# Kernel optimization log

Measured on AMD Instinct MI355X. Metric: run time of the kernel, lower is better.

## Reference

```python
import jax, jax.numpy as jnp
import numpy as np

NUM_HEADS = 4   # forced by reshape(B, N, num_heads, C) of a dim*4 projection
BN_EPS = 1e-5


def _chamfer(a, b):
    # a, b: [B, N, 3] -> symmetric chamfer distance (mean of nearest sq-dists)
    d = (jnp.sum(a ** 2, -1)[:, :, None] + jnp.sum(b ** 2, -1)[:, None, :]
         - 2.0 * jnp.einsum('bnc,bmc->bnm', a, b))
    return jnp.mean(jnp.min(d, axis=2)) + jnp.mean(jnp.min(d, axis=1))


def _forward(xs, pc1, bn_gamma, bn_beta, q_w, kv_w, proj_w, proj_b, map_w, map_b):
    B, F, C, N = xs.shape
    H = NUM_HEADS
    scale = C ** -0.5  # head_dim == dim in this module (full-dim heads)

    def per_item(x):  # x: [F, C, N]
        # BatchNorm1d in eval mode (running_mean=0, running_var=1)
        xn = (x / jnp.sqrt(1.0 + BN_EPS)) * bn_gamma[:, None] + bn_beta[:, None]
        xn = xn.transpose(0, 2, 1)                 # [F, N, C]
        xr = xn[::-1]                              # flip over frame axis
        q = (xn @ q_w.T).reshape(F, N, H, C).transpose(0, 2, 1, 3)        # [F,H,N,C]
        kv = (xr @ kv_w.T).reshape(F, N, 2, H, C).transpose(2, 0, 3, 1, 4)
        k, v = kv[0], kv[1]                        # [F,H,N,C]
        attn = jax.nn.softmax(jnp.einsum('fhnc,fhmc->fhnm', q, k) * scale, axis=-1)
        o = jnp.einsum('fhnm,fhmc->fhnc', attn, v).transpose(0, 2, 1, 3)  # [F,N,H,C]
        xa = (o[0] + o[1]).transpose(1, 0, 2)      # [H, N, C]: sum of first two frames
        xa = xa @ proj_w.T + proj_b                # [H, N, C] x_appearance
        fr = xa @ map_w.T + map_b                  # [H, N, 3] frames (mapping_xyz)
        return xa, fr

    xa, frames = jax.vmap(per_item)(xs)            # [B,H,N,C], [B,H,N,3]
    pc1t = pc1.transpose(0, 2, 1)                  # [B, N, 3]
    loss = _chamfer(pc1t + frames[:, 0], pc1t)
    return xa[:, 1:], frames[:, 1:], loss


def setup_inputs() -> dict:
    key = jax.random.key(0)
    ks = jax.random.split(key, 8)
    B, F, C, N = 2, 4, 64, 2048
    return {
        'xs': jax.random.normal(ks[0], (B, F, C, N), jnp.float32),
        'pc1': jax.random.normal(ks[1], (B, 3, N), jnp.float32),
        'pc2': jax.random.normal(ks[2], (B, 3, N), jnp.float32),
        'bn_gamma': jnp.ones((C,), jnp.float32),
        'bn_beta': jnp.zeros((C,), jnp.float32),
        'q_w': 0.02 * jax.random.normal(ks[3], (4 * C, C), jnp.float32),
        'kv_w': 0.02 * jax.random.normal(ks[4], (8 * C, C), jnp.float32),
        'proj_w': 0.02 * jax.random.normal(ks[5], (C, C), jnp.float32),
        'proj_b': jnp.zeros((C,), jnp.float32),
        'map_w': 0.02 * jax.random.normal(ks[6], (3, C), jnp.float32),
        'map_b': jnp.zeros((3,), jnp.float32),
    }


def reference(xs, pc1, pc2, bn_gamma, bn_beta, q_w, kv_w, proj_w, proj_b, map_w, map_b):
    # pc2 is accepted by the torch forward but unused in its body
    return _forward(xs, pc1, bn_gamma, bn_beta, q_w, kv_w, proj_w, proj_b, map_w, map_b)
```

## Files before the change

kernel.cpp:

```cpp
#include <hip/hip_runtime.h>
#include <hip/hip_bf16.h>

#define NPTS 2048
#define LOG2E 1.4426950408889634f
#define NJC 16
#define JCH 128

typedef short bf16x8 __attribute__((ext_vector_type(8)));
typedef float f32x4 __attribute__((ext_vector_type(4)));
typedef unsigned uint32x4 __attribute__((ext_vector_type(4)));
typedef __attribute__((address_space(3))) char lds_char;
typedef __attribute__((address_space(1))) const char glob_char;

union PBU { uint32x4 u; bf16x8 v; };

static __device__ __forceinline__ unsigned cvt_pk_bf16(float a, float b) {
    unsigned r;
    asm("v_cvt_pk_bf16_f32 %0, %1, %2" : "=v"(r) : "v"(a), "v"(b));
    return r;
}

__global__ void prep_weights(const float* __restrict__ gamma, const float* __restrict__ beta,
                             const float* __restrict__ q_w, const float* __restrict__ kv_w,
                             float* __restrict__ Wp, float* __restrict__ bp) {
    int j = blockIdx.x * blockDim.x + threadIdx.x;
    if (j >= 768) return;
    const float inv = 1.0f / sqrtf(1.0f + 1e-5f);
    const float* src;
    float scale;
    if (j < 256) { src = q_w + j * 64;          scale = 0.125f * LOG2E; }
    else         { src = kv_w + (j - 256) * 64; scale = 1.0f; }
    float b = 0.f;
    for (int c = 0; c < 64; ++c) {
        float w = src[c];
        Wp[j * 64 + c] = w * gamma[c] * inv * scale;
        b += w * beta[c];
    }
    bp[j] = b * scale;
}

__global__ __launch_bounds__(256) void qkv_gemm(const float* __restrict__ xs,
                                                const float* __restrict__ Wp,
                                                const float* __restrict__ bp,
                                                __hip_bfloat16* __restrict__ Qg,
                                                __hip_bfloat16* __restrict__ Kg,
                                                __hip_bfloat16* __restrict__ Vtg) {
    const int bf = blockIdx.z;
    const int b = bf >> 1, f01 = bf & 1;
    const int jt = blockIdx.y;
    const int f_src = (jt < 4) ? f01 : (3 - f01);
    const int n0 = blockIdx.x * 64;
    const float* __restrict__ A = xs + (size_t)((b * 4 + f_src) * 64) * NPTS;

    __shared__ float As[64][68];
    __shared__ float Ws[64][68];

    const int t = threadIdx.x;
    const int tx = t & 15, ty = t >> 4;

    for (int r = 0; r < 4; ++r) {
        int row = ty + 16 * r;
        int col = tx * 4;
        *(float4*)&As[row][col] = *(const float4*)&A[(size_t)row * NPTS + n0 + col];
        *(float4*)&Ws[row][col] = *(const float4*)&Wp[(size_t)(jt * 64 + row) * 64 + col];
    }
    __syncthreads();

    float acc[4][4];
#pragma unroll
    for (int jj = 0; jj < 4; ++jj) {
        float bv = bp[jt * 64 + tx + 16 * jj];
#pragma unroll
        for (int i = 0; i < 4; ++i) acc[i][jj] = bv;
    }
    for (int c = 0; c < 64; ++c) {
        float a[4], w[4];
#pragma unroll
        for (int i = 0; i < 4; ++i) a[i] = As[c][ty + 16 * i];
#pragma unroll
        for (int jj = 0; jj < 4; ++jj) w[jj] = Ws[tx + 16 * jj][c];
#pragma unroll
        for (int i = 0; i < 4; ++i)
#pragma unroll
            for (int jj = 0; jj < 4; ++jj) acc[i][jj] += a[i] * w[jj];
    }

    if (jt < 8) {
        __hip_bfloat16* __restrict__ dst = (jt < 4 ? Qg : Kg) + (size_t)bf * NPTS * 256;
        const int jb = (jt & 3) * 64;
#pragma unroll
        for (int i = 0; i < 4; ++i) {
            int n = n0 + ty + 16 * i;
#pragma unroll
            for (int jj = 0; jj < 4; ++jj)
                dst[(size_t)n * 256 + jb + tx + 16 * jj] = __float2bfloat16(acc[i][jj]);
        }
    } else {
        __syncthreads();
#pragma unroll
        for (int i = 0; i < 4; ++i)
#pragma unroll
            for (int jj = 0; jj < 4; ++jj)
                As[tx + 16 * jj][ty + 16 * i] = acc[i][jj];
        __syncthreads();
        const int row = t >> 2, c0 = (t & 3) * 16;
        __hip_bfloat16* __restrict__ dst =
            Vtg + ((size_t)bf * 256 + (jt - 8) * 64 + row) * NPTS + n0 + c0;
#pragma unroll
        for (int c = 0; c < 16; ++c) dst[c] = __float2bfloat16(As[row][c0 + c]);
    }
}

__global__ __launch_bounds__(256) void attn_mfma(const __hip_bfloat16* __restrict__ Qg,
                                                 const __hip_bfloat16* __restrict__ Kg,
                                                 const __hip_bfloat16* __restrict__ Vtg,
                                                 float* __restrict__ OT,
                                                 float* __restrict__ Lp) {
    const int combo = blockIdx.x;
    const int bf = combo >> 2, h = combo & 3;
    const int n0 = blockIdx.y * 64;
    const int split = blockIdx.z;
    const int kbase = split * (NPTS / 2);
    const int NT = NPTS / 2 / 64;

    __shared__ __align__(16) char smem[32768];

    const int t = threadIdx.x;
    const int lane = t & 63, w = t >> 6;
    const int l15 = lane & 15, g = lane >> 4;
    const int srow = lane >> 3, sslot = lane & 7;

    const __hip_bfloat16* qbase =
        Qg + ((size_t)bf * NPTS + n0 + w * 16 + l15) * 256 + h * 64 + g * 8;
    bf16x8 qf0 = *(const bf16x8*)(qbase);
    bf16x8 qf1 = *(const bf16x8*)(qbase + 32);

    const __hip_bfloat16* kgb = Kg + (size_t)bf * NPTS * 256 + h * 64;
    const __hip_bfloat16* vgb = Vtg + ((size_t)bf * 256 + h * 64) * NPTS;

    f32x4 oacc[4];
    float lsum = 0.f;
#pragma unroll
    for (int r = 0; r < 4; ++r) oacc[r] = (f32x4){0.f, 0.f, 0.f, 0.f};

    auto stage = [&](int kt, int bsel) {
#pragma unroll
        for (int ii = 0; ii < 2; ++ii) {
            const int rb = w * 16 + ii * 8;
            const int r = rb + srow;
            const int cs = (sslot ^ (r & 7)) * 8;
            const __hip_bfloat16* ksrc = kgb + (size_t)(kbase + kt * 64 + r) * 256 + cs;
            __builtin_amdgcn_global_load_lds((const glob_char*)ksrc,
                (lds_char*)(smem + bsel * 16384 + rb * 128), 16, 0, 0);
            const __hip_bfloat16* vsrc = vgb + (size_t)r * NPTS + kbase + kt * 64 + cs;
            __builtin_amdgcn_global_load_lds((const glob_char*)vsrc,
                (lds_char*)(smem + bsel * 16384 + 8192 + rb * 128), 16, 0, 0);
        }
    };

    stage(0, 0);
    int cur = 0;

    for (int kt = 0; kt < NT; ++kt) {
        if (kt < NT - 1) {
            stage(kt + 1, cur ^ 1);
            asm volatile("s_waitcnt vmcnt(4)" ::: "memory");
        } else {
            asm volatile("s_waitcnt vmcnt(0)" ::: "memory");
        }
        __builtin_amdgcn_s_barrier();
        asm volatile("" ::: "memory");

        char* const Kt = smem + cur * 16384;
        char* const Vt = Kt + 8192;

        f32x4 st[4];
#pragma unroll
        for (int tt = 0; tt < 4; ++tt) {
            const int row = tt * 16 + l15;
            bf16x8 kf0 = *(const bf16x8*)(Kt + row * 128 + ((g ^ (row & 7)) << 4));
            bf16x8 kf1 = *(const bf16x8*)(Kt + row * 128 + (((4 + g) ^ (row & 7)) << 4));
            f32x4 z = (f32x4){0.f, 0.f, 0.f, 0.f};
            z = __builtin_amdgcn_mfma_f32_16x16x32_bf16(kf0, qf0, z, 0, 0, 0);
            z = __builtin_amdgcn_mfma_f32_16x16x32_bf16(kf1, qf1, z, 0, 0, 0);
            st[tt] = z;
        }

        unsigned c0[4], c1[4];
#pragma unroll
        for (int tt = 0; tt < 4; ++tt) {
            float p0 = exp2f(fminf(st[tt][0], 126.f));
            float p1 = exp2f(fminf(st[tt][1], 126.f));
            float p2 = exp2f(fminf(st[tt][2], 126.f));
            float p3 = exp2f(fminf(st[tt][3], 126.f));
            lsum += (p0 + p1) + (p2 + p3);
            c0[tt] = cvt_pk_bf16(p0, p1);
            c1[tt] = cvt_pk_bf16(p2, p3);
        }

        bf16x8 pb[2];
#pragma unroll
        for (int s = 0; s < 2; ++s) {
            unsigned x0 = c0[2 * s], y0 = c0[2 * s + 1];
            unsigned x1 = c1[2 * s], y1 = c1[2 * s + 1];
            asm("v_permlane32_swap_b32 %0, %1" : "+v"(x0), "+v"(y0));
            asm("v_permlane16_swap_b32 %0, %1" : "+v"(x0), "+v"(y0));
            asm("v_permlane32_swap_b32 %0, %1" : "+v"(x1), "+v"(y1));
            asm("v_permlane16_swap_b32 %0, %1" : "+v"(x1), "+v"(y1));
            PBU pu;
            pu.u = (uint32x4){x0, x1, y0, y1};
            pb[s] = pu.v;
        }

#pragma unroll
        for (int ct = 0; ct < 4; ++ct) {
            const int row = ct * 16 + l15;
            bf16x8 vf0 = *(const bf16x8*)(Vt + row * 128 + ((g ^ (row & 7)) << 4));
            bf16x8 vf1 = *(const bf16x8*)(Vt + row * 128 + (((4 + g) ^ (row & 7)) << 4));
            f32x4 z = oacc[ct];
            z = __builtin_amdgcn_mfma_f32_16x16x32_bf16(vf0, pb[0], z, 0, 0, 0);
            z = __builtin_amdgcn_mfma_f32_16x16x32_bf16(vf1, pb[1], z, 0, 0, 0);
            oacc[ct] = z;
        }

        asm volatile("s_waitcnt lgkmcnt(0)" ::: "memory");
        __builtin_amdgcn_s_barrier();
        asm volatile("" ::: "memory");
        cur ^= 1;
    }

    lsum += __shfl_xor(lsum, 16);
    lsum += __shfl_xor(lsum, 32);
    const int q = n0 + w * 16 + l15;
    if (g == 0)
        Lp[(size_t)(split * 16 + combo) * NPTS + q] = lsum;

    float* __restrict__ Op = OT + (size_t)(split * 16 + combo) * 64 * NPTS;
#pragma unroll
    for (int ct = 0; ct < 4; ++ct)
#pragma unroll
        for (int r = 0; r < 4; ++r)
            Op[(size_t)(ct * 16 + g * 4 + r) * NPTS + q] = oacc[ct][r];
}

__global__ __launch_bounds__(256) void proj_frames(const float* __restrict__ OT,
                                                   const float* __restrict__ Lp,
                                                   const float* __restrict__ proj_w,
                                                   const float* __restrict__ proj_b,
                                                   const float* __restrict__ map_w,
                                                   const float* __restrict__ map_b,
                                                   float* __restrict__ out,
                                                   float* __restrict__ frames0) {
    const int bh = blockIdx.y, b = bh >> 2, h = bh & 3;
    const int n0 = blockIdx.x * 64;
    const int cf0 = (b * 2 + 0) * 4 + h;
    const int cf1 = (b * 2 + 1) * 4 + h;

    __shared__ float Xs[64][68];
    __shared__ float Ws[64][68];
    __shared__ float xaS[64][68];

    const int t = threadIdx.x;
    const int tx = t & 15, ty = t >> 4;
    const int nc = n0 + tx * 4;

    float4 la = *(const float4*)&Lp[(size_t)cf0 * NPTS + nc];
    float4 lb = *(const float4*)&Lp[(size_t)(16 + cf0) * NPTS + nc];
    float4 inv0 = make_float4(1.f / (la.x + lb.x), 1.f / (la.y + lb.y),
                              1.f / (la.z + lb.z), 1.f / (la.w + lb.w));
    la = *(const float4*)&Lp[(size_t)cf1 * NPTS + nc];
    lb = *(const float4*)&Lp[(size_t)(16 + cf1) * NPTS + nc];
    float4 inv1 = make_float4(1.f / (la.x + lb.x), 1.f / (la.y + lb.y),
                              1.f / (la.z + lb.z), 1.f / (la.w + lb.w));

    for (int r = 0; r < 4; ++r) {
        int row = ty + 16 * r, col = tx * 4;
        const float* p00 = OT + ((size_t)(cf0)      * 64 + row) * NPTS + n0 + col;
        const float* p01 = OT + ((size_t)(16 + cf0) * 64 + row) * NPTS + n0 + col;
        const float* p10 = OT + ((size_t)(cf1)      * 64 + row) * NPTS + n0 + col;
        const float* p11 = OT + ((size_t)(16 + cf1) * 64 + row) * NPTS + n0 + col;
        float4 a0 = *(const float4*)p00, a1 = *(const float4*)p01;
        float4 b0 = *(const float4*)p10, b1 = *(const float4*)p11;
        float4 x;
        x.x = (a0.x + a1.x) * inv0.x + (b0.x + b1.x) * inv1.x;
        x.y = (a0.y + a1.y) * inv0.y + (b0.y + b1.y) * inv1.y;
        x.z = (a0.z + a1.z) * inv0.z + (b0.z + b1.z) * inv1.z;
        x.w = (a0.w + a1.w) * inv0.w + (b0.w + b1.w) * inv1.w;
        *(float4*)&Xs[row][col] = x;
        *(float4*)&Ws[row][col] = *(const float4*)&proj_w[(size_t)row * 64 + col];
    }
    __syncthreads();

    float acc[4][4];
#pragma unroll
    for (int jj = 0; jj < 4; ++jj) {
        float bv = proj_b[tx + 16 * jj];
#pragma unroll
        for (int i = 0; i < 4; ++i) acc[i][jj] = bv;
    }
    for (int c = 0; c < 64; ++c) {
        float a[4], w[4];
#pragma unroll
        for (int i = 0; i < 4; ++i) a[i] = Xs[c][ty + 16 * i];
#pragma unroll
        for (int jj = 0; jj < 4; ++jj) w[jj] = Ws[tx + 16 * jj][c];
#pragma unroll
        for (int i = 0; i < 4; ++i)
#pragma unroll
            for (int jj = 0; jj < 4; ++jj) acc[i][jj] += a[i] * w[jj];
    }

#pragma unroll
    for (int i = 0; i < 4; ++i)
#pragma unroll
        for (int jj = 0; jj < 4; ++jj)
            xaS[ty + 16 * i][tx + 16 * jj] = acc[i][jj];

    if (h >= 1) {
        float* __restrict__ xa_out = out + (size_t)(b * 3 + h - 1) * NPTS * 64;
#pragma unroll
        for (int i = 0; i < 4; ++i)
#pragma unroll
            for (int jj = 0; jj < 4; ++jj)
                xa_out[(size_t)(n0 + ty + 16 * i) * 64 + tx + 16 * jj] = acc[i][jj];
    }
    __syncthreads();

    if (t < 192) {
        int r = t / 3, j = t % 3;
        float s = map_b[j];
        for (int c = 0; c < 64; ++c) s += xaS[r][c] * map_w[j * 64 + c];
        int n = n0 + r;
        if (h == 0) frames0[((size_t)b * NPTS + n) * 3 + j] = s;
        else        out[786432 + ((size_t)(b * 3 + h - 1) * NPTS + n) * 3 + j] = s;
    }
}

__global__ __launch_bounds__(256) void chamfer_partial(const float* __restrict__ pc1,
                                                       const float* __restrict__ frames0,
                                                       float* __restrict__ partial) {
    const int z = blockIdx.z;
    const int dir = z >> 1, b = z & 1;
    const int i = blockIdx.x * 256 + threadIdx.x;
    const int j0 = blockIdx.y * JCH;
    const float* __restrict__ px = pc1 + (size_t)b * 3 * NPTS;
    const float* __restrict__ fr = frames0 + (size_t)b * NPTS * 3;

    __shared__ float4 sj[JCH];
    if (threadIdx.x < JCH) {
        int jj = j0 + threadIdx.x;
        float bx = px[jj], by = px[NPTS + jj], bz = px[2 * NPTS + jj];
        if (dir == 1) { bx += fr[jj * 3]; by += fr[jj * 3 + 1]; bz += fr[jj * 3 + 2]; }
        sj[threadIdx.x] = make_float4(bx, by, bz, bx * bx + by * by + bz * bz);
    }
    float ax = px[i], ay = px[NPTS + i], az = px[2 * NPTS + i];
    if (dir == 0) { ax += fr[i * 3]; ay += fr[i * 3 + 1]; az += fr[i * 3 + 2]; }
    const float a2 = ax * ax + ay * ay + az * az;
    __syncthreads();

    float best = 1e30f;
#pragma unroll 4
    for (int k = 0; k < JCH; ++k) {
        float4 p = sj[k];
        float d = a2 + p.w - 2.0f * (ax * p.x + ay * p.y + az * p.z);
        best = fminf(best, d);
    }
    partial[((size_t)z * NJC + blockIdx.y) * NPTS + i] = best;
}

__global__ __launch_bounds__(256) void chamfer_minsum(const float* __restrict__ partial,
                                                      double* __restrict__ sums) {
    const int gid = blockIdx.x * 256 + threadIdx.x;
    const int z = gid >> 11, i = gid & 2047;
    float best = 1e30f;
#pragma unroll
    for (int c = 0; c < NJC; ++c)
        best = fminf(best, partial[((size_t)z * NJC + c) * NPTS + i]);
    __shared__ double sm[256];
    sm[threadIdx.x] = (double)best;
    __syncthreads();
    for (int off = 128; off > 0; off >>= 1) {
        if (threadIdx.x < off) sm[threadIdx.x] += sm[threadIdx.x + off];
        __syncthreads();
    }
    if (threadIdx.x == 0) sums[blockIdx.x] = sm[0];
}

__global__ void chamfer_final(const double* __restrict__ sums, float* __restrict__ loss_out) {
    if (threadIdx.x == 0) {
        double s = 0.0;
        for (int k = 0; k < 32; ++k) s += sums[k];
        loss_out[0] = (float)(s / 4096.0);
    }
}

extern "C" void kernel_launch(void* const* d_in, const int* in_sizes, int n_in,
                              void* d_out, int out_size, void* d_ws, size_t ws_size,
                              hipStream_t stream) {
    const float* xs     = (const float*)d_in[0];
    const float* pc1    = (const float*)d_in[1];
    const float* gamma  = (const float*)d_in[3];
    const float* beta   = (const float*)d_in[4];
    const float* q_w    = (const float*)d_in[5];
    const float* kv_w   = (const float*)d_in[6];
    const float* proj_w = (const float*)d_in[7];
    const float* proj_b = (const float*)d_in[8];
    const float* map_w  = (const float*)d_in[9];
    const float* map_b  = (const float*)d_in[10];
    float* out = (float*)d_out;

    char* ws = (char*)d_ws;
    __hip_bfloat16* Qg  = (__hip_bfloat16*)(ws);
    __hip_bfloat16* Kg  = (__hip_bfloat16*)(ws + 4194304);
    __hip_bfloat16* Vtg = (__hip_bfloat16*)(ws + 8388608);
    float* OT      = (float*)(ws + 12582912);
    float* Wp      = (float*)(ws + 29360128);
    float* bp      = (float*)(ws + 29556736);
    float* frames0 = (float*)(ws + 29559808);
    float* partial = (float*)(ws + 29609984);
    double* sums   = (double*)(ws + 30134272);
    float* Lp      = (float*)(ws + 30134528);

    hipLaunchKernelGGL(prep_weights, dim3(3), dim3(256), 0, stream,
                       gamma, beta, q_w, kv_w, Wp, bp);
    hipLaunchKernelGGL(qkv_gemm, dim3(32, 12, 4), dim3(256), 0, stream,
                       xs, Wp, bp, Qg, Kg, Vtg);
    hipLaunchKernelGGL(attn_mfma, dim3(16, 32, 2), dim3(256), 0, stream,
                       Qg, Kg, Vtg, OT, Lp);
    hipLaunchKernelGGL(proj_frames, dim3(32, 8), dim3(256), 0, stream,
                       OT, Lp, proj_w, proj_b, map_w, map_b, out, frames0);
    hipLaunchKernelGGL(chamfer_partial, dim3(NPTS / 256, NJC, 4), dim3(256), 0, stream,
                       pc1, frames0, partial);
    hipLaunchKernelGGL(chamfer_minsum, dim3(32), dim3(256), 0, stream,
                       partial, sums);
    hipLaunchKernelGGL(chamfer_final, dim3(1), dim3(64), 0, stream,
                       sums, out + 823296);
}
```

Baseline: 92.96 us.

## Double query tile per warp, split keys four ways, store attention partials in bf16

Each warp in the attention kernel now handles two 16-row query tiles, so every K/V tile loaded into LDS serves twice as many queries. The key range is split four ways instead of two to keep the grid size up. Partial outputs are written as bf16 instead of fp32, and proj_frames sums four partials. Other changes are precomputed LDS offsets, s_setprio around the MFMA blocks and a minimum of 4 blocks per CU in launch bounds. This cuts K/V staging traffic and partial-output bandwidth, at the cost of more registers and bf16 rounding of the unnormalized partial sums.

New measurement: 91.86 us. No clear change (-1.2%).

```diff
diff --git a/kernel.cpp b/kernel.cpp
--- a/kernel.cpp
+++ b/kernel.cpp
@@ -18,6 +18,9 @@
     unsigned r;
     asm("v_cvt_pk_bf16_f32 %0, %1, %2" : "=v"(r) : "v"(a), "v"(b));
     return r;
+}
+static __device__ __forceinline__ float b2f(unsigned short u) {
+    return __uint_as_float((unsigned)u << 16);
 }
 
 __global__ void prep_weights(const float* __restrict__ gamma, const float* __restrict__ beta,
@@ -111,17 +114,17 @@
     }
 }
 
-__global__ __launch_bounds__(256) void attn_mfma(const __hip_bfloat16* __restrict__ Qg,
-                                                 const __hip_bfloat16* __restrict__ Kg,
-                                                 const __hip_bfloat16* __restrict__ Vtg,
-                                                 float* __restrict__ OT,
-                                                 float* __restrict__ Lp) {
+__global__ __launch_bounds__(256, 4) void attn_mfma(const __hip_bfloat16* __restrict__ Qg,
+                                                    const __hip_bfloat16* __restrict__ Kg,
+                                                    const __hip_bfloat16* __restrict__ Vtg,
+                                                    __hip_bfloat16* __restrict__ OTb,
+                                                    float* __restrict__ Lp) {
     const int combo = blockIdx.x;
     const int bf = combo >> 2, h = combo & 3;
-    const int n0 = blockIdx.y * 64;
+    const int n0 = blockIdx.y * 128;
     const int split = blockIdx.z;
-    const int kbase = split * (NPTS / 2);
-    const int NT = NPTS / 2 / 64;
+    const int kbase = split * (NPTS / 4);
+    const int NT = NPTS / 4 / 64;
 
     __shared__ __align__(16) char smem[32768];
 
@@ -131,17 +134,31 @@
     const int srow = lane >> 3, sslot = lane & 7;
 
     const __hip_bfloat16* qbase =
-        Qg + ((size_t)bf * NPTS + n0 + w * 16 + l15) * 256 + h * 64 + g * 8;
-    bf16x8 qf0 = *(const bf16x8*)(qbase);
-    bf16x8 qf1 = *(const bf16x8*)(qbase + 32);
+        Qg + ((size_t)bf * NPTS + n0 + w * 32 + l15) * 256 + h * 64 + g * 8;
+    bf16x8 qf[2][2];
+    qf[0][0] = *(const bf16x8*)(qbase);
+    qf[0][1] = *(const bf16x8*)(qbase + 32);
+    qf[1][0] = *(const bf16x8*)(qbase + 16 * 256);
+    qf[1][1] = *(const bf16x8*)(qbase + 16 * 256 + 32);
 
     const __hip_bfloat16* kgb = Kg + (size_t)bf * NPTS * 256 + h * 64;
     const __hip_bfloat16* vgb = Vtg + ((size_t)bf * 256 + h * 64) * NPTS;
 
-    f32x4 oacc[4];
-    float lsum = 0.f;
-#pragma unroll
-    for (int r = 0; r < 4; ++r) oacc[r] = (f32x4){0.f, 0.f, 0.f, 0.f};
+    int ldsoff[4][2];
+#pragma unroll
+    for (int tt = 0; tt < 4; ++tt) {
+        const int row = tt * 16 + l15;
+#pragma unroll
+        for (int s = 0; s < 2; ++s)
+            ldsoff[tt][s] = row * 128 + (((s * 4 + g) ^ (row & 7)) << 4);
+    }
+
+    f32x4 oacc[2][4];
+    float lsum0 = 0.f, lsum1 = 0.f;
+#pragma unroll
+    for (int f = 0; f < 2; ++f)
+#pragma unroll
+        for (int r = 0; r < 4; ++r) oacc[f][r] = (f32x4){0.f, 0.f, 0.f, 0.f};
 
     auto stage = [&](int kt, int bsel) {
 #pragma unroll
@@ -171,57 +188,105 @@
         __builtin_amdgcn_s_barrier();
         asm volatile("" ::: "memory");
 
-        char* const Kt = smem + cur * 16384;
-        char* const Vt = Kt + 8192;
-
-        f32x4 st[4];
+        const char* Kt = smem + cur * 16384;
+        const char* Vt = Kt + 8192;
+
+        bf16x8 kf[4][2];
 #pragma unroll
         for (int tt = 0; tt < 4; ++tt) {
-            const int row = tt * 16 + l15;
-            bf16x8 kf0 = *(const bf16x8*)(Kt + row * 128 + ((g ^ (row & 7)) << 4));
-            bf16x8 kf1 = *(const bf16x8*)(Kt + row * 128 + (((4 + g) ^ (row & 7)) << 4));
-            f32x4 z = (f32x4){0.f, 0.f, 0.f, 0.f};
-            z = __builtin_amdgcn_mfma_f32_16x16x32_bf16(kf0, qf0, z, 0, 0, 0);
-            z = __builtin_amdgcn_mfma_f32_16x16x32_bf16(kf1, qf1, z, 0, 0, 0);
-            st[tt] = z;
-        }
-
-        unsigned c0[4], c1[4];
-#pragma unroll
-        for (int tt = 0; tt < 4; ++tt) {
-            float p0 = exp2f(fminf(st[tt][0], 126.f));
-            float p1 = exp2f(fminf(st[tt][1], 126.f));
-            float p2 = exp2f(fminf(st[tt][2], 126.f));
-            float p3 = exp2f(fminf(st[tt][3], 126.f));
-            lsum += (p0 + p1) + (p2 + p3);
-            c0[tt] = cvt_pk_bf16(p0, p1);
-            c1[tt] = cvt_pk_bf16(p2, p3);
-        }
-
-        bf16x8 pb[2];
-#pragma unroll
-        for (int s = 0; s < 2; ++s) {
-            unsigned x0 = c0[2 * s], y0 = c0[2 * s + 1];
-            unsigned x1 = c1[2 * s], y1 = c1[2 * s + 1];
-            asm("v_permlane32_swap_b32 %0, %1" : "+v"(x0), "+v"(y0));
-            asm("v_permlane16_swap_b32 %0, %1" : "+v"(x0), "+v"(y0));
-            asm("v_permlane32_swap_b32 %0, %1" : "+v"(x1), "+v"(y1));
-            asm("v_permlane16_swap_b32 %0, %1" : "+v"(x1), "+v"(y1));
-            PBU pu;
-            pu.u = (uint32x4){x0, x1, y0, y1};
-            pb[s] = pu.v;
-        }
-
+            kf[tt][0] = *(const bf16x8*)(Kt + ldsoff[tt][0]);
+            kf[tt][1] = *(const bf16x8*)(Kt + ldsoff[tt][1]);
+        }
+
+        bf16x8 pb0[2], pb1[2];
+
+        {
+            f32x4 st[4];
+            __builtin_amdgcn_s_setprio(1);
+#pragma unroll
+            for (int tt = 0; tt < 4; ++tt) {
+                f32x4 z = (f32x4){0.f, 0.f, 0.f, 0.f};
+                z = __builtin_amdgcn_mfma_f32_16x16x32_bf16(kf[tt][0], qf[0][0], z, 0, 0, 0);
+                z = __builtin_amdgcn_mfma_f32_16x16x32_bf16(kf[tt][1], qf[0][1], z, 0, 0, 0);
+                st[tt] = z;
+            }
+            __builtin_amdgcn_s_setprio(0);
+            unsigned c0[4], c1[4];
+#pragma unroll
+            for (int tt = 0; tt < 4; ++tt) {
+                float p0 = exp2f(fminf(st[tt][0], 126.f));
+                float p1 = exp2f(fminf(st[tt][1], 126.f));
+                float p2 = exp2f(fminf(st[tt][2], 126.f));
+                float p3 = exp2f(fminf(st[tt][3], 126.f));
+                lsum0 += (p0 + p1) + (p2 + p3);
+                c0[tt] = cvt_pk_bf16(p0, p1);
+                c1[tt] = cvt_pk_bf16(p2, p3);
+            }
+#pragma unroll
+            for (int s = 0; s < 2; ++s) {
+                unsigned x0 = c0[2 * s], y0 = c0[2 * s + 1];
+                unsigned x1 = c1[2 * s], y1 = c1[2 * s + 1];
+                asm("v_permlane32_swap_b32 %0, %1" : "+v"(x0), "+v"(y0));
+                asm("v_permlane16_swap_b32 %0, %1" : "+v"(x0), "+v"(y0));
+                asm("v_permlane32_swap_b32 %0, %1" : "+v"(x1), "+v"(y1));
+                asm("v_permlane16_swap_b32 %0, %1" : "+v"(x1), "+v"(y1));
+                PBU pu;
+                pu.u = (uint32x4){x0, x1, y0, y1};
+                pb0[s] = pu.v;
+            }
+        }
+
+        {
+            f32x4 st[4];
+            __builtin_amdgcn_s_setprio(1);
+#pragma unroll
+            for (int tt = 0; tt < 4; ++tt) {
+                f32x4 z = (f32x4){0.f, 0.f, 0.f, 0.f};
+                z = __builtin_amdgcn_mfma_f32_16x16x32_bf16(kf[tt][0], qf[1][0], z, 0, 0, 0);
+                z = __builtin_amdgcn_mfma_f32_16x16x32_bf16(kf[tt][1], qf[1][1], z, 0, 0, 0);
+                st[tt] = z;
+            }
+            __builtin_amdgcn_s_setprio(0);
+            unsigned c0[4], c1[4];
+#pragma unroll
+            for (int tt = 0; tt < 4; ++tt) {
+                float p0 = exp2f(fminf(st[tt][0], 126.f));
+                float p1 = exp2f(fminf(st[tt][1], 126.f));
+                float p2 = exp2f(fminf(st[tt][2], 126.f));
+                float p3 = exp2f(fminf(st[tt][3], 126.f));
+                lsum1 += (p0 + p1) + (p2 + p3);
+                c0[tt] = cvt_pk_bf16(p0, p1);
+                c1[tt] = cvt_pk_bf16(p2, p3);
+            }
+#pragma unroll
+            for (int s = 0; s < 2; ++s) {
+                unsigned x0 = c0[2 * s], y0 = c0[2 * s + 1];
+                unsigned x1 = c1[2 * s], y1 = c1[2 * s + 1];
+                asm("v_permlane32_swap_b32 %0, %1" : "+v"(x0), "+v"(y0));
+                asm("v_permlane16_swap_b32 %0, %1" : "+v"(x0), "+v"(y0));
+                asm("v_permlane32_swap_b32 %0, %1" : "+v"(x1), "+v"(y1));
+                asm("v_permlane16_swap_b32 %0, %1" : "+v"(x1), "+v"(y1));
+                PBU pu;
+                pu.u = (uint32x4){x0, x1, y0, y1};
+                pb1[s] = pu.v;
+            }
+        }
+
+        __builtin_amdgcn_s_setprio(1);
 #pragma unroll
         for (int ct = 0; ct < 4; ++ct) {
-            const int row = ct * 16 + l15;
-            bf16x8 vf0 = *(const bf16x8*)(Vt + row * 128 + ((g ^ (row & 7)) << 4));
-            bf16x8 vf1 = *(const bf16x8*)(Vt + row * 128 + (((4 + g) ^ (row & 7)) << 4));
-            f32x4 z = oacc[ct];
-            z = __builtin_amdgcn_mfma_f32_16x16x32_bf16(vf0, pb[0], z, 0, 0, 0);
-            z = __builtin_amdgcn_mfma_f32_16x16x32_bf16(vf1, pb[1], z, 0, 0, 0);
-            oacc[ct] = z;
-        }
+            bf16x8 vf0 = *(const bf16x8*)(Vt + ldsoff[ct][0]);
+            bf16x8 vf1 = *(const bf16x8*)(Vt + ldsoff[ct][1]);
+            f32x4 z0 = oacc[0][ct];
+            z0 = __builtin_amdgcn_mfma_f32_16x16x32_bf16(vf0, pb0[0], z0, 0, 0, 0);
+            z0 = __builtin_amdgcn_mfma_f32_16x16x32_bf16(vf1, pb0[1], z0, 0, 0, 0);
+            oacc[0][ct] = z0;
+            f32x4 z1 = oacc[1][ct];
+            z1 = __builtin_amdgcn_mfma_f32_16x16x32_bf16(vf0, pb1[0], z1, 0, 0, 0);
+            z1 = __builtin_amdgcn_mfma_f32_16x16x32_bf16(vf1, pb1[1], z1, 0, 0, 0);
+            oacc[1][ct] = z1;
+        }
+        __builtin_amdgcn_s_setprio(0);
 
         asm volatile("s_waitcnt lgkmcnt(0)" ::: "memory");
         __builtin_amdgcn_s_barrier();
@@ -229,21 +294,27 @@
         cur ^= 1;
     }
 
-    lsum += __shfl_xor(lsum, 16);
-    lsum += __shfl_xor(lsum, 32);
-    const int q = n0 + w * 16 + l15;
-    if (g == 0)
-        Lp[(size_t)(split * 16 + combo) * NPTS + q] = lsum;
-
-    float* __restrict__ Op = OT + (size_t)(split * 16 + combo) * 64 * NPTS;
+    lsum0 += __shfl_xor(lsum0, 16);
+    lsum0 += __shfl_xor(lsum0, 32);
+    lsum1 += __shfl_xor(lsum1, 16);
+    lsum1 += __shfl_xor(lsum1, 32);
+    const int qq = n0 + w * 32 + l15;
+    if (g == 0) {
+        Lp[(size_t)(split * 16 + combo) * NPTS + qq] = lsum0;
+        Lp[(size_t)(split * 16 + combo) * NPTS + qq + 16] = lsum1;
+    }
+
+    __hip_bfloat16* __restrict__ Op = OTb + (size_t)(split * 16 + combo) * 64 * NPTS;
 #pragma unroll
     for (int ct = 0; ct < 4; ++ct)
 #pragma unroll
-        for (int r = 0; r < 4; ++r)
-            Op[(size_t)(ct * 16 + g * 4 + r) * NPTS + q] = oacc[ct][r];
-}
-
-__global__ __launch_bounds__(256) void proj_frames(const float* __restrict__ OT,
+        for (int r = 0; r < 4; ++r) {
+            Op[(size_t)(ct * 16 + g * 4 + r) * NPTS + qq] = __float2bfloat16(oacc[0][ct][r]);
+            Op[(size_t)(ct * 16 + g * 4 + r) * NPTS + qq + 16] = __float2bfloat16(oacc[1][ct][r]);
+        }
+}
+
+__global__ __launch_bounds__(256) void proj_frames(const __hip_bfloat16* __restrict__ OTb,
                                                    const float* __restrict__ Lp,
                                                    const float* __restrict__ proj_w,
                                                    const float* __restrict__ proj_b,
@@ -264,29 +335,32 @@
     const int tx = t & 15, ty = t >> 4;
     const int nc = n0 + tx * 4;
 
-    float4 la = *(const float4*)&Lp[(size_t)cf0 * NPTS + nc];
-    float4 lb = *(const float4*)&Lp[(size_t)(16 + cf0) * NPTS + nc];
-    float4 inv0 = make_float4(1.f / (la.x + lb.x), 1.f / (la.y + lb.y),
-                              1.f / (la.z + lb.z), 1.f / (la.w + lb.w));
-    la = *(const float4*)&Lp[(size_t)cf1 * NPTS + nc];
-    lb = *(const float4*)&Lp[(size_t)(16 + cf1) * NPTS + nc];
-    float4 inv1 = make_float4(1.f / (la.x + lb.x), 1.f / (la.y + lb.y),
-                              1.f / (la.z + lb.z), 1.f / (la.w + lb.w));
+    float4 L0 = make_float4(0.f, 0.f, 0.f, 0.f), L1 = L0;
+#pragma unroll
+    for (int s = 0; s < 4; ++s) {
+        float4 a = *(const float4*)&Lp[(size_t)(s * 16 + cf0) * NPTS + nc];
+        L0.x += a.x; L0.y += a.y; L0.z += a.z; L0.w += a.w;
+        float4 c = *(const float4*)&Lp[(size_t)(s * 16 + cf1) * NPTS + nc];
+        L1.x += c.x; L1.y += c.y; L1.z += c.z; L1.w += c.w;
+    }
+    float4 inv0 = make_float4(1.f / L0.x, 1.f / L0.y, 1.f / L0.z, 1.f / L0.w);
+    float4 inv1 = make_float4(1.f / L1.x, 1.f / L1.y, 1.f / L1.z, 1.f / L1.w);
 
     for (int r = 0; r < 4; ++r) {
         int row = ty + 16 * r, col = tx * 4;
-        const float* p00 = OT + ((size_t)(cf0)      * 64 + row) * NPTS + n0 + col;
-        const float* p01 = OT + ((size_t)(16 + cf0) * 64 + row) * NPTS + n0 + col;
-        const float* p10 = OT + ((size_t)(cf1)      * 64 + row) * NPTS + n0 + col;
-        const float* p11 = OT + ((size_t)(16 + cf1) * 64 + row) * NPTS + n0 + col;
-        float4 a0 = *(const float4*)p00, a1 = *(const float4*)p01;
-        float4 b0 = *(const float4*)p10, b1 = *(const float4*)p11;
-        float4 x;
-        x.x = (a0.x + a1.x) * inv0.x + (b0.x + b1.x) * inv1.x;
-        x.y = (a0.y + a1.y) * inv0.y + (b0.y + b1.y) * inv1.y;
-        x.z = (a0.z + a1.z) * inv0.z + (b0.z + b1.z) * inv1.z;
-        x.w = (a0.w + a1.w) * inv0.w + (b0.w + b1.w) * inv1.w;
-        *(float4*)&Xs[row][col] = x;
+        float x0 = 0.f, x1 = 0.f, x2 = 0.f, x3 = 0.f;
+        float y0 = 0.f, y1 = 0.f, y2 = 0.f, y3 = 0.f;
+#pragma unroll
+        for (int s = 0; s < 4; ++s) {
+            ushort4 u0 = *(const ushort4*)&OTb[((size_t)(s * 16 + cf0) * 64 + row) * NPTS + n0 + col];
+            ushort4 u1 = *(const ushort4*)&OTb[((size_t)(s * 16 + cf1) * 64 + row) * NPTS + n0 + col];
+            x0 += b2f(u0.x); x1 += b2f(u0.y); x2 += b2f(u0.z); x3 += b2f(u0.w);
+            y0 += b2f(u1.x); y1 += b2f(u1.y); y2 += b2f(u1.z); y3 += b2f(u1.w);
+        }
+        Xs[row][col + 0] = x0 * inv0.x + y0 * inv1.x;
+        Xs[row][col + 1] = x1 * inv0.y + y1 * inv1.y;
+        Xs[row][col + 2] = x2 * inv0.z + y2 * inv1.z;
+        Xs[row][col + 3] = x3 * inv0.w + y3 * inv1.w;
         *(float4*)&Ws[row][col] = *(const float4*)&proj_w[(size_t)row * 64 + col];
     }
     __syncthreads();
@@ -413,7 +487,7 @@
     __hip_bfloat16* Qg  = (__hip_bfloat16*)(ws);
     __hip_bfloat16* Kg  = (__hip_bfloat16*)(ws + 4194304);
     __hip_bfloat16* Vtg = (__hip_bfloat16*)(ws + 8388608);
-    float* OT      = (float*)(ws + 12582912);
+    __hip_bfloat16* OTb = (__hip_bfloat16*)(ws + 12582912);
     float* Wp      = (float*)(ws + 29360128);
     float* bp      = (float*)(ws + 29556736);
     float* frames0 = (float*)(ws + 29559808);
@@ -425,10 +499,10 @@
                        gamma, beta, q_w, kv_w, Wp, bp);
     hipLaunchKernelGGL(qkv_gemm, dim3(32, 12, 4), dim3(256), 0, stream,
                        xs, Wp, bp, Qg, Kg, Vtg);
-    hipLaunchKernelGGL(attn_mfma, dim3(16, 32, 2), dim3(256), 0, stream,
-                       Qg, Kg, Vtg, OT, Lp);
+    hipLaunchKernelGGL(attn_mfma, dim3(16, 16, 4), dim3(256), 0, stream,
+                       Qg, Kg, Vtg, OTb, Lp);
     hipLaunchKernelGGL(proj_frames, dim3(32, 8), dim3(256), 0, stream,
-                       OT, Lp, proj_w, proj_b, map_w, map_b, out, frames0);
+                       OTb, Lp, proj_w, proj_b, map_w, map_b, out, frames0);
     hipLaunchKernelGGL(chamfer_partial, dim3(NPTS / 256, NJC, 4), dim3(256), 0, stream,
                        pc1, frames0, partial);
     hipLaunchKernelGGL(chamfer_minsum, dim3(32), dim3(256), 0, stream,
```
